# Kernel tuning notes

Measured on AMD Instinct MI355X. Metric: run time of the kernel, lower is better.

The kernel has to match this reference:

```python
import jax, jax.numpy as jnp
import numpy as np
import math

H = 512
N2 = 32  # N // 2
L_VAL = 4096

def setup_inputs() -> dict:
    key = jax.random.key(0)
    kC, = jax.random.split(key, 1)
    alpha = math.pi
    # Faithful to original init
    log_dt = jnp.full((H,), math.log(1e-4), dtype=jnp.float32)
    A_imag = jnp.broadcast_to(jnp.arange(N2, dtype=jnp.float32) * alpha, (H, N2))
    A_imag = A_imag.at[:, 0].set(0.0)
    log_A_real = jnp.full((H, N2), math.log(3.0), dtype=jnp.float32)
    log_A_real = log_A_real.at[:, 0].set(-5.0)
    C_cplx = (jax.random.normal(kC, (H, N2, 2), dtype=jnp.float32))
    scale = (jnp.abs(A_imag) / 1000.0)[..., None]
    C = C_cplx * scale  # real view of complex C, shape (H, N2, 2)
    return {"L": L_VAL, "C": C, "log_dt": log_dt, "log_A_real": log_A_real, "A_imag": A_imag}

def reference(L, C, log_dt, log_A_real, A_imag):
    dt = jnp.exp(log_dt)                                  # (H,)
    Cc = C[..., 0] + 1j * C[..., 1]                       # (H, N2) complex
    A = -jnp.exp(log_A_real) + 1j * A_imag                # (H, N2)
    dtA = A * dt[:, None]                                 # (H, N2)
    # Vandermonde: exp(dtA * l) for l in [0, L)
    Kexp = jnp.exp(dtA[..., None] * jnp.arange(L, dtype=jnp.float32))  # (H, N2, L)
    Ceff = Cc * (jnp.exp(dtA) - 1.0) / A                  # (H, N2)
    K = 2.0 * jnp.einsum('hn,hnl->hl', Ceff, Kexp).real    # (H, L)
    return K
```

## Files before the change

### kernel.cpp

```cpp
#include <hip/hip_runtime.h>
#include <math.h>

#define N2V 32
#define BLOCK 512
#define CHUNK 4096

typedef float v2f __attribute__((ext_vector_type(2)));

__global__ __launch_bounds__(BLOCK) void s4d_vand_kernel(
    const float* __restrict__ C,
    const float* __restrict__ log_dt,
    const float* __restrict__ log_A_real,
    const float* __restrict__ A_imag,
    float* __restrict__ K,
    int L, int chunks_per_h)
{
    __shared__ float4 sC[N2V];
    __shared__ float2 sP[N2V][64];
    __shared__ float4 sQre[N2V][16];
    __shared__ float4 sQim[N2V][16];

    const int h     = blockIdx.x / chunks_per_h;
    const int chunk = (blockIdx.x % chunks_per_h) * CHUNK;
    const int t     = threadIdx.x;

    if (t < N2V) {
        const int n = t;
        const float dt = expf(log_dt[h]);
        const float ar = -expf(log_A_real[h * N2V + n]);
        const float ai = A_imag[h * N2V + n];
        const float x = ar * dt;
        const float y = ai * dt;
        float sn, cs;
        sincosf(y, &sn, &cs);
        const float e  = expf(x);
        const float wr = e * cs - 1.0f;
        const float wi = e * sn;
        const float inv = 1.0f / (ar * ar + ai * ai);
        const float dr = (wr * ar + wi * ai) * inv;
        const float di = (wi * ar - wr * ai) * inv;
        const float cr = C[(h * N2V + n) * 2 + 0];
        const float ci = C[(h * N2V + n) * 2 + 1];
        sC[n] = make_float4(x, y,
                            2.0f * (cr * dr - ci * di),
                            2.0f * (cr * di + ci * dr));
    }
    __syncthreads();

#pragma unroll
    for (int i = 0; i < 4; ++i) {
        const int e = t + i * BLOCK;
        const int n = e >> 6;
        const int b = e & 63;
        const float4 c = sC[n];
        const float fb = (float)b;
        float sn, cs;
        __sincosf(c.y * fb, &sn, &cs);
        const float ex = __expf(c.x * fb);
        sP[n][b] = make_float2(ex * (c.z * cs - c.w * sn),
                               ex * (c.z * sn + c.w * cs));
    }
    {
        const int n = t >> 4;
        const int k = t & 15;
        const float4 c = sC[n];
        float re[4], im[4];
#pragma unroll
        for (int j = 0; j < 4; ++j) {
            const float fl = (float)(chunk + 64 * (4 * k + j));
            float sn, cs;
            __sincosf(c.y * fl, &sn, &cs);
            const float ex = __expf(c.x * fl);
            re[j] = ex * cs;
            im[j] = -ex * sn;
        }
        sQre[n][k] = make_float4(re[0], re[1], re[2], re[3]);
        sQim[n][k] = make_float4(im[0], im[1], im[2], im[3]);
    }
    __syncthreads();

    const int b = t & 63;
    const int w = t >> 6;

    v2f acc[4];
#pragma unroll
    for (int j = 0; j < 4; ++j) acc[j] = (v2f){0.0f, 0.0f};

#pragma unroll 2
    for (int n = 0; n < N2V; ++n) {
        const float2 p   = sP[n][b];
        const float4 re0 = sQre[n][2 * w];
        const float4 re1 = sQre[n][2 * w + 1];
        const float4 im0 = sQim[n][2 * w];
        const float4 im1 = sQim[n][2 * w + 1];
        const v2f px = {p.x, p.x};
        const v2f py = {p.y, p.y};
        acc[0] = __builtin_elementwise_fma(px, (v2f){re0.x, re0.y},
                 __builtin_elementwise_fma(py, (v2f){im0.x, im0.y}, acc[0]));
        acc[1] = __builtin_elementwise_fma(px, (v2f){re0.z, re0.w},
                 __builtin_elementwise_fma(py, (v2f){im0.z, im0.w}, acc[1]));
        acc[2] = __builtin_elementwise_fma(px, (v2f){re1.x, re1.y},
                 __builtin_elementwise_fma(py, (v2f){im1.x, im1.y}, acc[2]));
        acc[3] = __builtin_elementwise_fma(px, (v2f){re1.z, re1.w},
                 __builtin_elementwise_fma(py, (v2f){im1.z, im1.w}, acc[3]));
    }

    float* out = K + (size_t)h * L + chunk + b;
#pragma unroll
    for (int j = 0; j < 4; ++j) {
        const int a0 = 8 * w + 2 * j;
        const int l0 = chunk + 64 * a0 + b;
        if (l0 < L)      out[(size_t)64 * a0]       = acc[j].x;
        if (l0 + 64 < L) out[(size_t)64 * (a0 + 1)] = acc[j].y;
    }
}

extern "C" void kernel_launch(void* const* d_in, const int* in_sizes, int n_in,
                              void* d_out, int out_size, void* d_ws, size_t ws_size,
                              hipStream_t stream) {
    const float* C          = (const float*)d_in[1];
    const float* log_dt     = (const float*)d_in[2];
    const float* log_A_real = (const float*)d_in[3];
    const float* A_imag     = (const float*)d_in[4];
    float* K = (float*)d_out;

    const int H = in_sizes[2];
    const int L = out_size / H;
    const int chunks_per_h = (L + CHUNK - 1) / CHUNK;

    dim3 grid(H * chunks_per_h);
    dim3 block(BLOCK);
    s4d_vand_kernel<<<grid, block, 0, stream>>>(C, log_dt, log_A_real, A_imag,
                                                K, L, chunks_per_h);
}
```

Measured before the change: 13.55 us.

## Halve block size, pair adjacent outputs per lane with float2 stores

Block size drops from 512 to 256 threads, and each lane now computes two adjacent output positions (2i, 2i+1). It does this by storing a pair of prefactors per (n, i) as a float4, derived with one extra complex multiply by exp(dtA). The coarse factor table moves to a 128-stride grid and each thread accumulates 8 packed pairs, which allows vectorized float2 global stores. The intent is fewer transcendental evaluations per output, wider stores, and more work per thread. In exchange it raises register pressure and halves the threads per block.

```diff
diff --git a/kernel.cpp b/kernel.cpp
--- a/kernel.cpp
+++ b/kernel.cpp
@@ -2,7 +2,7 @@
 #include <math.h>
 
 #define N2V 32
-#define BLOCK 512
+#define BLOCK 256
 #define CHUNK 4096
 
 typedef float v2f __attribute__((ext_vector_type(2)));
@@ -16,9 +16,10 @@
     int L, int chunks_per_h)
 {
     __shared__ float4 sC[N2V];
-    __shared__ float2 sP[N2V][64];
-    __shared__ float4 sQre[N2V][16];
-    __shared__ float4 sQim[N2V][16];
+    __shared__ float2 sR[N2V];
+    __shared__ float4 sP4[N2V][64];
+    __shared__ float  sQre[N2V][32];
+    __shared__ float  sQim[N2V][32];
 
     const int h     = blockIdx.x / chunks_per_h;
     const int chunk = (blockIdx.x % chunks_per_h) * CHUNK;
@@ -44,74 +45,87 @@
         sC[n] = make_float4(x, y,
                             2.0f * (cr * dr - ci * di),
                             2.0f * (cr * di + ci * dr));
+        sR[n] = make_float2(e * cs, e * sn);
     }
     __syncthreads();
 
 #pragma unroll
-    for (int i = 0; i < 4; ++i) {
-        const int e = t + i * BLOCK;
+    for (int m = 0; m < 8; ++m) {
+        const int e = t + m * BLOCK;
         const int n = e >> 6;
-        const int b = e & 63;
+        const int i = e & 63;
         const float4 c = sC[n];
-        const float fb = (float)b;
+        const float2 r = sR[n];
+        const float fb = (float)(2 * i);
         float sn, cs;
         __sincosf(c.y * fb, &sn, &cs);
         const float ex = __expf(c.x * fb);
-        sP[n][b] = make_float2(ex * (c.z * cs - c.w * sn),
-                               ex * (c.z * sn + c.w * cs));
+        const float ur = ex * cs, ui = ex * sn;
+        const float p0r = c.z * ur - c.w * ui;
+        const float p0i = c.z * ui + c.w * ur;
+        const float p1r = p0r * r.x - p0i * r.y;
+        const float p1i = p0r * r.y + p0i * r.x;
+        sP4[n][i] = make_float4(p0r, p1r, p0i, p1i);
     }
-    {
-        const int n = t >> 4;
-        const int k = t & 15;
+#pragma unroll
+    for (int m = 0; m < 4; ++m) {
+        const int e = t + m * BLOCK;
+        const int n = e >> 5;
+        const int a = e & 31;
         const float4 c = sC[n];
-        float re[4], im[4];
-#pragma unroll
-        for (int j = 0; j < 4; ++j) {
-            const float fl = (float)(chunk + 64 * (4 * k + j));
-            float sn, cs;
-            __sincosf(c.y * fl, &sn, &cs);
-            const float ex = __expf(c.x * fl);
-            re[j] = ex * cs;
-            im[j] = -ex * sn;
-        }
-        sQre[n][k] = make_float4(re[0], re[1], re[2], re[3]);
-        sQim[n][k] = make_float4(im[0], im[1], im[2], im[3]);
+        const float fl = (float)(chunk + 128 * a);
+        float sn, cs;
+        __sincosf(c.y * fl, &sn, &cs);
+        const float ex = __expf(c.x * fl);
+        sQre[n][a] =  ex * cs;
+        sQim[n][a] = -ex * sn;
     }
     __syncthreads();
 
-    const int b = t & 63;
-    const int w = t >> 6;
+    const int lane = t & 63;
+    const int w    = t >> 6;
 
-    v2f acc[4];
+    v2f acc[8];
 #pragma unroll
-    for (int j = 0; j < 4; ++j) acc[j] = (v2f){0.0f, 0.0f};
+    for (int j = 0; j < 8; ++j) acc[j] = (v2f){0.0f, 0.0f};
 
 #pragma unroll 2
     for (int n = 0; n < N2V; ++n) {
-        const float2 p   = sP[n][b];
-        const float4 re0 = sQre[n][2 * w];
-        const float4 re1 = sQre[n][2 * w + 1];
-        const float4 im0 = sQim[n][2 * w];
-        const float4 im1 = sQim[n][2 * w + 1];
-        const v2f px = {p.x, p.x};
-        const v2f py = {p.y, p.y};
-        acc[0] = __builtin_elementwise_fma(px, (v2f){re0.x, re0.y},
-                 __builtin_elementwise_fma(py, (v2f){im0.x, im0.y}, acc[0]));
-        acc[1] = __builtin_elementwise_fma(px, (v2f){re0.z, re0.w},
-                 __builtin_elementwise_fma(py, (v2f){im0.z, im0.w}, acc[1]));
-        acc[2] = __builtin_elementwise_fma(px, (v2f){re1.x, re1.y},
-                 __builtin_elementwise_fma(py, (v2f){im1.x, im1.y}, acc[2]));
-        acc[3] = __builtin_elementwise_fma(px, (v2f){re1.z, re1.w},
-                 __builtin_elementwise_fma(py, (v2f){im1.z, im1.w}, acc[3]));
+        const float4 pp = sP4[n][lane];
+        const float4* q4r = (const float4*)&sQre[n][0];
+        const float4* q4i = (const float4*)&sQim[n][0];
+        const float4 qr0 = q4r[2 * w];
+        const float4 qr1 = q4r[2 * w + 1];
+        const float4 qi0 = q4i[2 * w];
+        const float4 qi1 = q4i[2 * w + 1];
+        const v2f prr = {pp.x, pp.y};
+        const v2f pii = {pp.z, pp.w};
+        acc[0] = __builtin_elementwise_fma(prr, (v2f){qr0.x, qr0.x},
+                 __builtin_elementwise_fma(pii, (v2f){qi0.x, qi0.x}, acc[0]));
+        acc[1] = __builtin_elementwise_fma(prr, (v2f){qr0.y, qr0.y},
+                 __builtin_elementwise_fma(pii, (v2f){qi0.y, qi0.y}, acc[1]));
+        acc[2] = __builtin_elementwise_fma(prr, (v2f){qr0.z, qr0.z},
+                 __builtin_elementwise_fma(pii, (v2f){qi0.z, qi0.z}, acc[2]));
+        acc[3] = __builtin_elementwise_fma(prr, (v2f){qr0.w, qr0.w},
+                 __builtin_elementwise_fma(pii, (v2f){qi0.w, qi0.w}, acc[3]));
+        acc[4] = __builtin_elementwise_fma(prr, (v2f){qr1.x, qr1.x},
+                 __builtin_elementwise_fma(pii, (v2f){qi1.x, qi1.x}, acc[4]));
+        acc[5] = __builtin_elementwise_fma(prr, (v2f){qr1.y, qr1.y},
+                 __builtin_elementwise_fma(pii, (v2f){qi1.y, qi1.y}, acc[5]));
+        acc[6] = __builtin_elementwise_fma(prr, (v2f){qr1.z, qr1.z},
+                 __builtin_elementwise_fma(pii, (v2f){qi1.z, qi1.z}, acc[6]));
+        acc[7] = __builtin_elementwise_fma(prr, (v2f){qr1.w, qr1.w},
+                 __builtin_elementwise_fma(pii, (v2f){qi1.w, qi1.w}, acc[7]));
     }
 
-    float* out = K + (size_t)h * L + chunk + b;
+    float* out = K + (size_t)h * L + chunk + 2 * lane;
 #pragma unroll
-    for (int j = 0; j < 4; ++j) {
-        const int a0 = 8 * w + 2 * j;
-        const int l0 = chunk + 64 * a0 + b;
-        if (l0 < L)      out[(size_t)64 * a0]       = acc[j].x;
-        if (l0 + 64 < L) out[(size_t)64 * (a0 + 1)] = acc[j].y;
+    for (int j = 0; j < 8; ++j) {
+        const int a  = 8 * w + j;
+        const int l0 = chunk + 2 * lane + 128 * a;
+        if (l0 < L)
+            *reinterpret_cast<float2*>(out + (size_t)128 * a) =
+                make_float2(acc[j].x, acc[j].y);
     }
 }
 
```

Result: slower. 15.82 us (+16.8%).
